# Optimization experiments

Measured on AMD Instinct MI355X. Metric: run time of the kernel, lower is better.

The kernel has to match this reference:

```python
import jax, jax.numpy as jnp
import numpy as np

D_MODEL = 96
D_STATE = 1
D_CONV = 3
SSM_RATIO = 2.0
D_INNER = int(D_MODEL * SSM_RATIO)   # 192
DT_RANK = int(np.ceil(D_MODEL / 16))  # 6
K = 4                                 # scan directions
BSZ, H, W = 4, 128, 128


def setup_inputs() -> dict:
    key = jax.random.key(0)
    ks = jax.random.split(key, 8)
    x = jax.random.normal(ks[0], (BSZ, D_MODEL, H, W), jnp.float32)
    in_w = jax.random.normal(ks[1], (D_INNER, D_MODEL), jnp.float32) * (D_MODEL ** -0.5)
    in_b = jnp.zeros((D_INNER,), jnp.float32)
    dw_w = jax.random.normal(ks[2], (D_INNER, 1, D_CONV, D_CONV), jnp.float32) * (1.0 / D_CONV)
    dw_b = jnp.zeros((D_INNER,), jnp.float32)
    x_proj_weight = jax.random.normal(ks[3], (K, DT_RANK + 2 * D_STATE, D_INNER), jnp.float32) * 0.02
    dt_projs_weight = jax.random.normal(ks[4], (K, D_INNER, DT_RANK), jnp.float32) * (DT_RANK ** -0.5)
    # mamba dt init: bias = softplus^{-1}(dt), dt ~ U[dt_min, dt_max]
    dt = jax.random.uniform(ks[5], (K, D_INNER), jnp.float32, 0.001, 0.1)
    dt_projs_bias = jnp.log(jnp.expm1(dt))
    A_logs = jnp.zeros((K * D_INNER, D_STATE), jnp.float32)  # log(arange(1,N+1)), N=1 -> 0
    Ds = jnp.ones((K * D_INNER,), jnp.float32)
    ln_w = jnp.ones((D_INNER,), jnp.float32)
    ln_b = jnp.zeros((D_INNER,), jnp.float32)
    out_w = jax.random.normal(ks[6], (D_MODEL, D_INNER), jnp.float32) * (D_INNER ** -0.5)
    out_b = jnp.zeros((D_MODEL,), jnp.float32)
    return {"x": x, "in_w": in_w, "in_b": in_b, "dw_w": dw_w, "dw_b": dw_b,
            "x_proj_weight": x_proj_weight, "dt_projs_weight": dt_projs_weight,
            "dt_projs_bias": dt_projs_bias, "A_logs": A_logs, "Ds": Ds,
            "ln_w": ln_w, "ln_b": ln_b, "out_w": out_w, "out_b": out_b}


def _forward(x, in_w, in_b, dw_w, dw_b, x_proj_weight, dt_projs_weight,
             dt_projs_bias, A_logs, Ds, ln_w, ln_b, out_w, out_b):
    B = x.shape[0]
    L = H * W
    # ---- in_proj: 1x1 conv -> depthwise conv -> SiLU ----
    z = jnp.einsum('bchw,dc->bdhw', x, in_w) + in_b[None, :, None, None]
    z = jax.lax.conv_general_dilated(z, dw_w, (1, 1), 'SAME',
                                     feature_group_count=D_INNER,
                                     dimension_numbers=('NCHW', 'OIHW', 'NCHW'))
    z = z + dw_b[None, :, None, None]
    z = z * jax.nn.sigmoid(z)  # SiLU
    # ---- cross scan: 4 directions [B,K,D,L] ----
    x0 = z.reshape(B, D_INNER, L)                          # row-major
    x1 = jnp.swapaxes(z, 2, 3).reshape(B, D_INNER, L)      # column-major
    xs = jnp.stack([x0, x1, jnp.flip(x0, -1), jnp.flip(x1, -1)], axis=1)
    # ---- x_proj (grouped 1x1 conv over L) ----
    x_dbl = jnp.einsum('bkdl,ked->bkel', xs, x_proj_weight)  # e = R + 2N
    dts_r = x_dbl[:, :, :DT_RANK]                            # [B,K,R,L]
    Bs = x_dbl[:, :, DT_RANK:DT_RANK + D_STATE]              # [B,K,N,L]
    Cs = x_dbl[:, :, DT_RANK + D_STATE:]                     # [B,K,N,L]
    dts = jnp.einsum('bkrl,kdr->bkdl', dts_r, dt_projs_weight)
    # ---- selective scan (fp32, delta_softplus=True) ----
    delta = jax.nn.softplus(dts + dt_projs_bias[None, :, :, None])     # [B,K,D,L]
    A = -jnp.exp(A_logs.astype(jnp.float32)).reshape(K, D_INNER, D_STATE)
    dA = jnp.exp(delta[..., None] * A[None, :, :, None, :])            # [B,K,D,L,N]
    Bt = jnp.swapaxes(Bs, 2, 3)                                        # [B,K,L,N]
    dBu = delta[..., None] * Bt[:, :, None] * xs[..., None]            # [B,K,D,L,N]

    def combine(c1, c2):
        a1, b1 = c1
        a2, b2 = c2
        return a1 * a2, b1 * a2 + b2

    _, hs = jax.lax.associative_scan(combine, (dA, dBu), axis=3)       # h_t states
    Ct = jnp.swapaxes(Cs, 2, 3)                                        # [B,K,L,N]
    y = jnp.einsum('bkdln,bkln->bkdl', hs, Ct) \
        + Ds.reshape(K, D_INNER)[None, :, :, None] * xs
    # ---- cross merge (inverse of cross scan, summed) ----
    y0 = y[:, 0]
    y1 = jnp.swapaxes(y[:, 1].reshape(B, D_INNER, W, H), 2, 3).reshape(B, D_INNER, L)
    y2 = jnp.flip(y[:, 2], -1)
    y3 = jnp.swapaxes(jnp.flip(y[:, 3], -1).reshape(B, D_INNER, W, H), 2, 3).reshape(B, D_INNER, L)
    ym = (y0 + y1 + y2 + y3).reshape(B, D_INNER, H, W).astype(x.dtype)
    # ---- out_proj: LayerNorm2d (over channels) + 1x1 conv ----
    yn = jnp.moveaxis(ym, 1, -1)  # [B,H,W,C]
    mu = yn.mean(-1, keepdims=True)
    var = yn.var(-1, keepdims=True)
    yn = (yn - mu) * jax.lax.rsqrt(var + 1e-5) * ln_w + ln_b
    yn = jnp.moveaxis(yn, -1, 1)
    return jnp.einsum('bdhw,cd->bchw', yn, out_w) + out_b[None, :, None, None]


def reference(x, in_w, in_b, dw_w, dw_b, x_proj_weight, dt_projs_weight,
              dt_projs_bias, A_logs, Ds, ln_w, ln_b, out_w, out_b):
    return _forward(x, in_w, in_b, dw_w, dw_b, x_proj_weight, dt_projs_weight,
                    dt_projs_bias, A_logs, Ds, ln_w, ln_b, out_w, out_b)
```

## Files before the change

kernel.cpp:

```cpp
#include <hip/hip_runtime.h>
#include <math.h>

#define D_MODEL 96
#define D_INNER 192
#define DT_RANK 6
#define K4      4
#define BSZ     4
#define HH      128
#define WW      128
#define LL      16384

#define LOG2E 1.4426950408889634f
#define LN2   0.6931471805599453f

#if __has_builtin(__builtin_amdgcn_exp2f)
__device__ __forceinline__ float fexp2_(float x){ return __builtin_amdgcn_exp2f(x); }
#else
__device__ __forceinline__ float fexp2_(float x){ return exp2f(x); }
#endif
#if __has_builtin(__builtin_amdgcn_logf)
__device__ __forceinline__ float flog2_(float x){ return __builtin_amdgcn_logf(x); }
#else
__device__ __forceinline__ float flog2_(float x){ return log2f(x); }
#endif
#if __has_builtin(__builtin_amdgcn_rcpf)
__device__ __forceinline__ float frcp_(float x){ return __builtin_amdgcn_rcpf(x); }
#else
__device__ __forceinline__ float frcp_(float x){ return 1.0f/x; }
#endif

__device__ __forceinline__ float softplus_fast(float x){
    return fmaxf(x, 0.0f) + LN2 * flog2_(1.0f + fexp2_(-LOG2E * fabsf(x)));
}
__device__ __forceinline__ float silu_fast(float x){
    return x * frcp_(1.0f + fexp2_(-LOG2E * x));
}

__global__ __launch_bounds__(256) void k_inproj(const float* __restrict__ x,
                                                const float* __restrict__ in_w,
                                                const float* __restrict__ in_b,
                                                float* __restrict__ z0) {
    const int blk = blockIdx.x;
    const int b  = blk >> 8;
    const int l0 = (blk & 255) << 6;
    const int p = threadIdx.x & 63;
    const int g = __builtin_amdgcn_readfirstlane(threadIdx.x >> 6);
    const float* xb = x + (size_t)b * D_MODEL * LL + l0 + p;
    float* zb = z0 + (size_t)b * D_INNER * LL + l0 + p;
    for (int jb = 0; jb < 6; ++jb) {
        const int d0 = g * 48 + jb * 8;
        float acc[8];
        #pragma unroll
        for (int j = 0; j < 8; ++j) acc[j] = in_b[d0 + j];
        const float* w0 = in_w + (size_t)d0 * D_MODEL;
        #pragma unroll 4
        for (int c = 0; c < D_MODEL; ++c) {
            float v = xb[(size_t)c * LL];
            #pragma unroll
            for (int j = 0; j < 8; ++j)
                acc[j] = fmaf(w0[c + j * D_MODEL], v, acc[j]);
        }
        #pragma unroll
        for (int j = 0; j < 8; ++j) zb[(size_t)(d0 + j) * LL] = acc[j];
    }
}

__global__ __launch_bounds__(256) void k_dwconv(const float* __restrict__ z0,
                                                const float* __restrict__ dw_w,
                                                const float* __restrict__ dw_b,
                                                float* __restrict__ z,
                                                float* __restrict__ zT) {
    __shared__ float tin[34][34];
    __shared__ float tout[32][33];
    const int blk  = blockIdx.x;
    const int tile = blk & 15;
    const int bd   = blk >> 4;
    const int d    = bd % D_INNER;
    const int h0 = (tile >> 2) << 5, w0 = (tile & 3) << 5;
    const float* src = z0 + (size_t)bd * LL;
    for (int i = threadIdx.x; i < 34 * 34; i += 256) {
        int r = i / 34, c = i - r * 34;
        int hh = h0 + r - 1, ww = w0 + c - 1;
        float v = 0.0f;
        if (hh >= 0 && hh < HH && ww >= 0 && ww < WW) v = src[hh * WW + ww];
        tin[r][c] = v;
    }
    __syncthreads();
    float wreg[9];
    #pragma unroll
    for (int i = 0; i < 9; ++i) wreg[i] = dw_w[d * 9 + i];
    const float bias = dw_b[d];
    #pragma unroll
    for (int i = 0; i < 4; ++i) {
        int idx = threadIdx.x + i * 256;
        int r = idx >> 5, c = idx & 31;
        float acc = bias;
        #pragma unroll
        for (int ky = 0; ky < 3; ++ky)
            #pragma unroll
            for (int kx = 0; kx < 3; ++kx)
                acc = fmaf(wreg[ky * 3 + kx], tin[r + ky][c + kx], acc);
        acc = silu_fast(acc);
        tout[r][c] = acc;
        z[(size_t)bd * LL + (h0 + r) * WW + w0 + c] = acc;
    }
    __syncthreads();
    #pragma unroll
    for (int i = 0; i < 4; ++i) {
        int idx = threadIdx.x + i * 256;
        int r = idx >> 5, c = idx & 31;
        zT[(size_t)bd * LL + (w0 + r) * HH + h0 + c] = tout[c][r];
    }
}

__global__ __launch_bounds__(256) void k_proj(const float* __restrict__ z,
                                              const float* __restrict__ zT,
                                              const float* __restrict__ xpw,
                                              float* __restrict__ dtsr,
                                              float* __restrict__ Bs,
                                              float* __restrict__ Cs) {
    const int blk = blockIdx.x;
    const int seg = blk >> 10;
    const int rest = blk & 1023;
    const int b  = rest >> 8;
    const int l0 = (rest & 255) << 6;
    const int kA = seg ? 1 : 0;
    const int kB = seg ? 3 : 2;
    const float* src = seg ? zT : z;
    const int p = threadIdx.x & 63;
    const int g = __builtin_amdgcn_readfirstlane(threadIdx.x >> 6);
    const float* sb = src + (size_t)b * D_INNER * LL + l0 + p;
    const int k  = (g < 2) ? kA : kB;
    const int e0 = (g & 1) * 4;
    const float* wrow = xpw + (size_t)(k * 8 + e0) * D_INNER;
    float a0 = 0.f, a1 = 0.f, a2 = 0.f, a3 = 0.f;
    #pragma unroll 4
    for (int dd = 0; dd < D_INNER; ++dd) {
        float v = sb[(size_t)dd * LL];
        a0 = fmaf(wrow[dd],               v, a0);
        a1 = fmaf(wrow[dd + D_INNER],     v, a1);
        a2 = fmaf(wrow[dd + 2 * D_INNER], v, a2);
        a3 = fmaf(wrow[dd + 3 * D_INNER], v, a3);
    }
    const int l = l0 + p;
    const size_t dbase = ((size_t)(b * K4 + k) * DT_RANK) * LL;
    if (e0 == 0) {
        dtsr[dbase + 0 * LL + l] = a0;
        dtsr[dbase + 1 * LL + l] = a1;
        dtsr[dbase + 2 * LL + l] = a2;
        dtsr[dbase + 3 * LL + l] = a3;
    } else {
        dtsr[dbase + 4 * LL + l] = a0;
        dtsr[dbase + 5 * LL + l] = a1;
        Bs[(size_t)(b * K4 + k) * LL + l] = a2;
        Cs[(size_t)(b * K4 + k) * LL + l] = a3;
    }
}

template <bool FWD, bool RMW, bool LDSU>
__device__ __forceinline__ void scan_core(const float* __restrict__ u_lin,
                                          const float* __restrict__ u_rm,
                                          const float* __restrict__ dtsr_k,
                                          const float* __restrict__ B_k,
                                          const float* __restrict__ C_k,
                                          const float* __restrict__ w6p,
                                          float dtbv, float A2, float Dval,
                                          float* __restrict__ dst,
                                          float* __restrict__ wPs,
                                          float* __restrict__ wSs,
                                          float* __restrict__ tile) {
    const int tid  = threadIdx.x;
    const int lane = tid & 63;
    const int wv   = tid >> 6;
    float w6[6];
    #pragma unroll
    for (int r = 0; r < 6; ++r) w6[r] = w6p[r];
    float h0 = 0.0f;
    for (int ci = 0; ci < 8; ++ci) {
        const int c  = FWD ? ci : (7 - ci);
        const int l0 = (c << 11) + (tid << 3);
        float u[8];
        if (LDSU) {
            #pragma unroll
            for (int e = 0; e < 8; ++e) {
                int idx = tid + (e << 8);
                int h = idx >> 4, w = idx & 15;
                tile[w * 132 + h] = u_rm[h * WW + (c << 4) + w];
            }
            __syncthreads();
            const int wl = tid >> 4;
            const int hb = (tid & 15) << 3;
            #pragma unroll
            for (int e = 0; e < 8; ++e) u[e] = tile[wl * 132 + hb + e];
        } else {
            float4 t0 = *(const float4*)(u_lin + l0);
            float4 t1 = *(const float4*)(u_lin + l0 + 4);
            u[0]=t0.x; u[1]=t0.y; u[2]=t0.z; u[3]=t0.w;
            u[4]=t1.x; u[5]=t1.y; u[6]=t1.z; u[7]=t1.w;
        }
        float dl[8];
        #pragma unroll
        for (int e = 0; e < 8; ++e) dl[e] = dtbv;
        #pragma unroll
        for (int r = 0; r < 6; ++r) {
            float4 t0 = *(const float4*)(dtsr_k + (size_t)r * LL + l0);
            float4 t1 = *(const float4*)(dtsr_k + (size_t)r * LL + l0 + 4);
            dl[0] = fmaf(w6[r], t0.x, dl[0]); dl[1] = fmaf(w6[r], t0.y, dl[1]);
            dl[2] = fmaf(w6[r], t0.z, dl[2]); dl[3] = fmaf(w6[r], t0.w, dl[3]);
            dl[4] = fmaf(w6[r], t1.x, dl[4]); dl[5] = fmaf(w6[r], t1.y, dl[5]);
            dl[6] = fmaf(w6[r], t1.z, dl[6]); dl[7] = fmaf(w6[r], t1.w, dl[7]);
        }
        float Bv[8], Cv[8];
        {
            float4 t0 = *(const float4*)(B_k + l0);
            float4 t1 = *(const float4*)(B_k + l0 + 4);
            Bv[0]=t0.x; Bv[1]=t0.y; Bv[2]=t0.z; Bv[3]=t0.w;
            Bv[4]=t1.x; Bv[5]=t1.y; Bv[6]=t1.z; Bv[7]=t1.w;
            t0 = *(const float4*)(C_k + l0);
            t1 = *(const float4*)(C_k + l0 + 4);
            Cv[0]=t0.x; Cv[1]=t0.y; Cv[2]=t0.z; Cv[3]=t0.w;
            Cv[4]=t1.x; Cv[5]=t1.y; Cv[6]=t1.z; Cv[7]=t1.w;
        }
        float a[8], bb[8];
        #pragma unroll
        for (int e = 0; e < 8; ++e) {
            float d1 = softplus_fast(dl[e]);
            a[e]  = fexp2_(d1 * A2);
            bb[e] = d1 * Bv[e] * u[e];
        }
        float P = 1.0f, S = 0.0f;
        if (FWD) {
            #pragma unroll
            for (int e = 0; e < 8; ++e) { S = fmaf(S, a[e], bb[e]); P *= a[e]; }
        } else {
            #pragma unroll
            for (int e = 7; e >= 0; --e) { S = fmaf(S, a[e], bb[e]); P *= a[e]; }
        }
        #pragma unroll
        for (int s = 1; s < 64; s <<= 1) {
            float p2, s2;
            if (FWD) { p2 = __shfl_up(P, s);   s2 = __shfl_up(S, s); }
            else     { p2 = __shfl_down(P, s); s2 = __shfl_down(S, s); }
            const bool act = FWD ? (lane >= s) : (lane + s < 64);
            if (act) { S = fmaf(s2, P, S); P = p2 * P; }
        }
        __syncthreads();
        if ((FWD && lane == 63) || (!FWD && lane == 0)) { wPs[wv] = P; wSs[wv] = S; }
        __syncthreads();
        float Pw = 1.0f, Sw = 0.0f;
        if (FWD) { for (int w2 = 0; w2 < wv; ++w2)  { Sw = fmaf(Sw, wPs[w2], wSs[w2]); Pw *= wPs[w2]; } }
        else     { for (int w2 = 3; w2 > wv; --w2)  { Sw = fmaf(Sw, wPs[w2], wSs[w2]); Pw *= wPs[w2]; } }
        float Pex, Sex;
        if (FWD) { Pex = __shfl_up(P, 1);   Sex = __shfl_up(S, 1);   if (lane == 0)  { Pex = 1.0f; Sex = 0.0f; } }
        else     { Pex = __shfl_down(P, 1); Sex = __shfl_down(S, 1); if (lane == 63) { Pex = 1.0f; Sex = 0.0f; } }
        float h = fmaf(Pw, h0, Sw);
        h = fmaf(Pex, h, Sex);
        float Pt = 1.0f, St = 0.0f;
        if (FWD) { for (int w2 = 0; w2 < 4; ++w2)  { St = fmaf(St, wPs[w2], wSs[w2]); Pt *= wPs[w2]; } }
        else     { for (int w2 = 3; w2 >= 0; --w2) { St = fmaf(St, wPs[w2], wSs[w2]); Pt *= wPs[w2]; } }
        h0 = fmaf(Pt, h0, St);
        float y[8];
        if (FWD) {
            #pragma unroll
            for (int e = 0; e < 8; ++e) { h = fmaf(a[e], h, bb[e]); y[e] = fmaf(h, Cv[e], Dval * u[e]); }
        } else {
            #pragma unroll
            for (int e = 7; e >= 0; --e) { h = fmaf(a[e], h, bb[e]); y[e] = fmaf(h, Cv[e], Dval * u[e]); }
        }
        if (!RMW) {
            *(float4*)(dst + l0)     = make_float4(y[0], y[1], y[2], y[3]);
            *(float4*)(dst + l0 + 4) = make_float4(y[4], y[5], y[6], y[7]);
        } else {
            float4 o0 = *(const float4*)(dst + l0);
            float4 o1 = *(const float4*)(dst + l0 + 4);
            o0.x += y[0]; o0.y += y[1]; o0.z += y[2]; o0.w += y[3];
            o1.x += y[4]; o1.y += y[5]; o1.z += y[6]; o1.w += y[7];
            *(float4*)(dst + l0)     = o0;
            *(float4*)(dst + l0 + 4) = o1;
        }
    }
}

__global__ __launch_bounds__(256) void k_scanA(const float* __restrict__ z,
                                               float* __restrict__ zT,
                                               float* __restrict__ y_r,
                                               const float* __restrict__ dtsr,
                                               const float* __restrict__ Bs,
                                               const float* __restrict__ Cs,
                                               const float* __restrict__ dtw,
                                               const float* __restrict__ dtb,
                                               const float* __restrict__ A_logs,
                                               const float* __restrict__ Ds) {
    __shared__ float wPs[4], wSs[4];
    const int blk = blockIdx.x;
    const int half = blk >= 768;
    const int bd = half ? blk - 768 : blk;
    const int b = bd / D_INNER, d = bd - b * D_INNER;
    const int k = half ? 3 : 0;
    const int kd = k * D_INNER + d;
    const float* dk = dtsr + ((size_t)(b * K4 + k) * DT_RANK) * LL;
    const float* Bk = Bs + (size_t)(b * K4 + k) * LL;
    const float* Ck = Cs + (size_t)(b * K4 + k) * LL;
    const float* w6p = dtw + (size_t)kd * 6;
    const float A2 = -expf(A_logs[kd]) * LOG2E;
    if (!half)
        scan_core<true, false, false>(z + (size_t)bd * LL, nullptr, dk, Bk, Ck, w6p,
                                      dtb[kd], A2, Ds[kd], y_r + (size_t)bd * LL,
                                      wPs, wSs, nullptr);
    else
        scan_core<false, false, false>(zT + (size_t)bd * LL, nullptr, dk, Bk, Ck, w6p,
                                       dtb[kd], A2, Ds[kd], zT + (size_t)bd * LL,
                                       wPs, wSs, nullptr);
}

__global__ __launch_bounds__(256) void k_scanB(const float* __restrict__ z,
                                               float* __restrict__ zT,
                                               float* __restrict__ y_r,
                                               const float* __restrict__ dtsr,
                                               const float* __restrict__ Bs,
                                               const float* __restrict__ Cs,
                                               const float* __restrict__ dtw,
                                               const float* __restrict__ dtb,
                                               const float* __restrict__ A_logs,
                                               const float* __restrict__ Ds) {
    __shared__ float wPs[4], wSs[4];
    __shared__ float tile[16 * 132];
    const int blk = blockIdx.x;
    const int half = blk >= 768;
    const int bd = half ? blk - 768 : blk;
    const int b = bd / D_INNER, d = bd - b * D_INNER;
    const int k = half ? 1 : 2;
    const int kd = k * D_INNER + d;
    const float* dk = dtsr + ((size_t)(b * K4 + k) * DT_RANK) * LL;
    const float* Bk = Bs + (size_t)(b * K4 + k) * LL;
    const float* Ck = Cs + (size_t)(b * K4 + k) * LL;
    const float* w6p = dtw + (size_t)kd * 6;
    const float A2 = -expf(A_logs[kd]) * LOG2E;
    if (!half)
        scan_core<false, true, false>(z + (size_t)bd * LL, nullptr, dk, Bk, Ck, w6p,
                                      dtb[kd], A2, Ds[kd], y_r + (size_t)bd * LL,
                                      wPs, wSs, nullptr);
    else
        scan_core<true, true, true>(nullptr, z + (size_t)bd * LL, dk, Bk, Ck, w6p,
                                    dtb[kd], A2, Ds[kd], zT + (size_t)bd * LL,
                                    wPs, wSs, tile);
}

__global__ __launch_bounds__(256) void k_taddT(const float* __restrict__ ym2,
                                               float* __restrict__ ym) {
    __shared__ float t[32][33];
    const int blk  = blockIdx.x;
    const int tile = blk & 15;
    const int bd   = blk >> 4;
    const int h0 = (tile >> 2) << 5, w0 = (tile & 3) << 5;
    const float* s = ym2 + (size_t)bd * LL;
    float* o = ym + (size_t)bd * LL;
    for (int i = threadIdx.x; i < 1024; i += 256) {
        int r = i >> 5, c = i & 31;
        t[r][c] = s[(w0 + r) * HH + h0 + c];
    }
    __syncthreads();
    for (int i = threadIdx.x; i < 1024; i += 256) {
        int r = i >> 5, c = i & 31;
        o[(h0 + r) * WW + w0 + c] += t[c][r];
    }
}

__global__ __launch_bounds__(256) void k_lnout(const float* __restrict__ ym,
                                               const float* __restrict__ ln_w,
                                               const float* __restrict__ ln_b,
                                               const float* __restrict__ out_w,
                                               const float* __restrict__ out_b,
                                               float* __restrict__ out) {
    const int blk = blockIdx.x;
    const int b  = blk >> 8;
    const int l0 = (blk & 255) << 6;
    const int p = threadIdx.x & 63;
    const int q = __builtin_amdgcn_readfirstlane(threadIdx.x >> 6);
    const float* vm = ym + (size_t)b * D_INNER * LL + l0 + p;
    float s1a = 0.f, s1b = 0.f, s2a = 0.f, s2b = 0.f;
    #pragma unroll 4
    for (int dd = 0; dd < D_INNER; dd += 2) {
        float v0 = vm[(size_t)dd * LL];
        float v1 = vm[(size_t)(dd + 1) * LL];
        s1a += v0; s2a = fmaf(v0, v0, s2a);
        s1b += v1; s2b = fmaf(v1, v1, s2b);
    }
    const float mu = (s1a + s1b) * (1.0f / 192.0f);
    const float var = (s2a + s2b) * (1.0f / 192.0f) - mu * mu;
    const float rs = rsqrtf(var + 1e-5f);
    float acc[24];
    #pragma unroll
    for (int cb = 0; cb < 24; ++cb) acc[cb] = 0.f;
    const float* wq = out_w + (size_t)q * 24 * D_INNER;
    #pragma unroll 4
    for (int dd = 0; dd < D_INNER; ++dd) {
        float v = vm[(size_t)dd * LL];
        float yn = fmaf((v - mu) * rs, ln_w[dd], ln_b[dd]);
        #pragma unroll
        for (int cb = 0; cb < 24; ++cb)
            acc[cb] = fmaf(wq[(size_t)cb * D_INNER + dd], yn, acc[cb]);
    }
    float* ob = out + (size_t)b * D_MODEL * LL + l0 + p;
    #pragma unroll
    for (int cb = 0; cb < 24; ++cb) {
        int cc = q * 24 + cb;
        ob[(size_t)cc * LL] = acc[cb] + out_b[cc];
    }
}

extern "C" void kernel_launch(void* const* d_in, const int* in_sizes, int n_in,
                              void* d_out, int out_size, void* d_ws, size_t ws_size,
                              hipStream_t stream) {
    (void)in_sizes; (void)n_in; (void)out_size; (void)ws_size;
    const float* x      = (const float*)d_in[0];
    const float* in_w   = (const float*)d_in[1];
    const float* in_b   = (const float*)d_in[2];
    const float* dw_w   = (const float*)d_in[3];
    const float* dw_b   = (const float*)d_in[4];
    const float* xpw    = (const float*)d_in[5];
    const float* dtw    = (const float*)d_in[6];
    const float* dtb    = (const float*)d_in[7];
    const float* A_logs = (const float*)d_in[8];
    const float* Ds     = (const float*)d_in[9];
    const float* ln_w   = (const float*)d_in[10];
    const float* ln_b   = (const float*)d_in[11];
    const float* out_w  = (const float*)d_in[12];
    const float* out_b  = (const float*)d_in[13];
    float* out = (float*)d_out;

    float* ws = (float*)d_ws;
    const size_t A1 = (size_t)BSZ * D_INNER * LL;
    float* z0   = ws;
    float* z    = ws + A1;
    float* zT   = ws + 2 * A1;
    float* dtsr = ws + 3 * A1;
    float* BsP  = dtsr + (size_t)BSZ * K4 * DT_RANK * LL;
    float* CsP  = BsP + (size_t)BSZ * K4 * LL;

    float* y_r = z0;

    k_inproj<<<1024, 256, 0, stream>>>(x, in_w, in_b, z0);
    k_dwconv<<<BSZ * D_INNER * 16, 256, 0, stream>>>(z0, dw_w, dw_b, z, zT);
    k_proj<<<2048, 256, 0, stream>>>(z, zT, xpw, dtsr, BsP, CsP);
    k_scanA<<<1536, 256, 0, stream>>>(z, zT, y_r, dtsr, BsP, CsP, dtw, dtb, A_logs, Ds);
    k_scanB<<<1536, 256, 0, stream>>>(z, zT, y_r, dtsr, BsP, CsP, dtw, dtb, A_logs, Ds);
    k_taddT<<<BSZ * D_INNER * 16, 256, 0, stream>>>(zT, y_r);
    k_lnout<<<1024, 256, 0, stream>>>(y_r, ln_w, ln_b, out_w, out_b, out);
}
```

Measured before the change: 437.2 us.

## Widen in_proj accumulators and split LN/out_proj across 8 waves

k_inproj now computes all 48 output channels per wave in a single pass, so each x value is loaded once instead of six times. That cuts global reads at the cost of many more live registers. k_lnout moves to 512 threads: the LayerNorm statistics are computed as per-wave partial sums over 24 channels and reduced through shared memory, and each wave computes 12 output channels instead of 24. This adds a block barrier and more redundant activation reads in exchange for more parallelism and fewer registers per thread. The k_proj unroll factor is raised from 4 to 8.

```diff
diff --git a/kernel.cpp b/kernel.cpp
--- a/kernel.cpp
+++ b/kernel.cpp
@@ -47,22 +47,20 @@
     const int g = __builtin_amdgcn_readfirstlane(threadIdx.x >> 6);
     const float* xb = x + (size_t)b * D_MODEL * LL + l0 + p;
     float* zb = z0 + (size_t)b * D_INNER * LL + l0 + p;
-    for (int jb = 0; jb < 6; ++jb) {
-        const int d0 = g * 48 + jb * 8;
-        float acc[8];
-        #pragma unroll
-        for (int j = 0; j < 8; ++j) acc[j] = in_b[d0 + j];
-        const float* w0 = in_w + (size_t)d0 * D_MODEL;
-        #pragma unroll 4
-        for (int c = 0; c < D_MODEL; ++c) {
-            float v = xb[(size_t)c * LL];
-            #pragma unroll
-            for (int j = 0; j < 8; ++j)
-                acc[j] = fmaf(w0[c + j * D_MODEL], v, acc[j]);
-        }
-        #pragma unroll
-        for (int j = 0; j < 8; ++j) zb[(size_t)(d0 + j) * LL] = acc[j];
-    }
+    const int d0 = g * 48;
+    float acc[48];
+    #pragma unroll
+    for (int j = 0; j < 48; ++j) acc[j] = in_b[d0 + j];
+    const float* w0 = in_w + (size_t)d0 * D_MODEL;
+    #pragma unroll 4
+    for (int c = 0; c < D_MODEL; ++c) {
+        float v = xb[(size_t)c * LL];
+        #pragma unroll
+        for (int j = 0; j < 48; ++j)
+            acc[j] = fmaf(w0[j * D_MODEL + c], v, acc[j]);
+    }
+    #pragma unroll
+    for (int j = 0; j < 48; ++j) zb[(size_t)(d0 + j) * LL] = acc[j];
 }
 
 __global__ __launch_bounds__(256) void k_dwconv(const float* __restrict__ z0,
@@ -134,7 +132,7 @@
     const int e0 = (g & 1) * 4;
     const float* wrow = xpw + (size_t)(k * 8 + e0) * D_INNER;
     float a0 = 0.f, a1 = 0.f, a2 = 0.f, a3 = 0.f;
-    #pragma unroll 4
+    #pragma unroll 8
     for (int dd = 0; dd < D_INNER; ++dd) {
         float v = sb[(size_t)dd * LL];
         a0 = fmaf(wrow[dd],               v, a0);
@@ -366,45 +364,51 @@
     }
 }
 
-__global__ __launch_bounds__(256) void k_lnout(const float* __restrict__ ym,
+__global__ __launch_bounds__(512) void k_lnout(const float* __restrict__ ym,
                                                const float* __restrict__ ln_w,
                                                const float* __restrict__ ln_b,
                                                const float* __restrict__ out_w,
                                                const float* __restrict__ out_b,
                                                float* __restrict__ out) {
+    __shared__ float red1[8][64];
+    __shared__ float red2[8][64];
     const int blk = blockIdx.x;
     const int b  = blk >> 8;
     const int l0 = (blk & 255) << 6;
     const int p = threadIdx.x & 63;
-    const int q = __builtin_amdgcn_readfirstlane(threadIdx.x >> 6);
+    const int g = __builtin_amdgcn_readfirstlane(threadIdx.x >> 6);
     const float* vm = ym + (size_t)b * D_INNER * LL + l0 + p;
-    float s1a = 0.f, s1b = 0.f, s2a = 0.f, s2b = 0.f;
-    #pragma unroll 4
-    for (int dd = 0; dd < D_INNER; dd += 2) {
-        float v0 = vm[(size_t)dd * LL];
-        float v1 = vm[(size_t)(dd + 1) * LL];
-        s1a += v0; s2a = fmaf(v0, v0, s2a);
-        s1b += v1; s2b = fmaf(v1, v1, s2b);
-    }
-    const float mu = (s1a + s1b) * (1.0f / 192.0f);
-    const float var = (s2a + s2b) * (1.0f / 192.0f) - mu * mu;
-    const float rs = rsqrtf(var + 1e-5f);
-    float acc[24];
-    #pragma unroll
-    for (int cb = 0; cb < 24; ++cb) acc[cb] = 0.f;
-    const float* wq = out_w + (size_t)q * 24 * D_INNER;
-    #pragma unroll 4
+    float s1 = 0.f, s2 = 0.f;
+    #pragma unroll 8
+    for (int j = 0; j < 24; ++j) {
+        float v = vm[(size_t)(g * 24 + j) * LL];
+        s1 += v;
+        s2 = fmaf(v, v, s2);
+    }
+    red1[g][p] = s1;
+    red2[g][p] = s2;
+    __syncthreads();
+    float t1 = 0.f, t2 = 0.f;
+    #pragma unroll
+    for (int j = 0; j < 8; ++j) { t1 += red1[j][p]; t2 += red2[j][p]; }
+    const float mu = t1 * (1.0f / 192.0f);
+    const float rs = rsqrtf(t2 * (1.0f / 192.0f) - mu * mu + 1e-5f);
+    float acc[12];
+    #pragma unroll
+    for (int cb = 0; cb < 12; ++cb) acc[cb] = 0.f;
+    const float* wq = out_w + (size_t)g * 12 * D_INNER;
+    #pragma unroll 8
     for (int dd = 0; dd < D_INNER; ++dd) {
         float v = vm[(size_t)dd * LL];
         float yn = fmaf((v - mu) * rs, ln_w[dd], ln_b[dd]);
         #pragma unroll
-        for (int cb = 0; cb < 24; ++cb)
+        for (int cb = 0; cb < 12; ++cb)
             acc[cb] = fmaf(wq[(size_t)cb * D_INNER + dd], yn, acc[cb]);
     }
     float* ob = out + (size_t)b * D_MODEL * LL + l0 + p;
     #pragma unroll
-    for (int cb = 0; cb < 24; ++cb) {
-        int cc = q * 24 + cb;
+    for (int cb = 0; cb < 12; ++cb) {
+        int cc = g * 12 + cb;
         ob[(size_t)cc * LL] = acc[cb] + out_b[cc];
     }
 }
@@ -446,5 +450,5 @@
     k_scanA<<<1536, 256, 0, stream>>>(z, zT, y_r, dtsr, BsP, CsP, dtw, dtb, A_logs, Ds);
     k_scanB<<<1536, 256, 0, stream>>>(z, zT, y_r, dtsr, BsP, CsP, dtw, dtb, A_logs, Ds);
     k_taddT<<<BSZ * D_INNER * 16, 256, 0, stream>>>(zT, y_r);
-    k_lnout<<<1024, 256, 0, stream>>>(y_r, ln_w, ln_b, out_w, out_b, out);
-}
+    k_lnout<<<1024, 512, 0, stream>>>(y_r, ln_w, ln_b, out_w, out_b, out);
+}
```

New measurement: 448.4 us. 2.6% more time.
